# Performance work log

Measured on AMD Instinct MI355X. Metric: run time of the kernel, lower is better.

The kernel has to match this reference:

```python
import jax, jax.numpy as jnp
import numpy as np

B, S, H = 32, 256, 128
K, C, DSUB, O = 8, 4096, 16, 6  # PQ subspaces, ncentroids=4096, subvector dim, bits/symbol


def setup_inputs() -> dict:
    key = jax.random.key(0)
    ks = jax.random.split(key, 8)
    return {
        "z": jax.random.normal(ks[0], (B, S, 3), jnp.float32),
        "W1": jax.random.normal(ks[1], (3, H), jnp.float32) * 0.3,
        "b1": jax.random.normal(ks[2], (H,), jnp.float32) * 0.1,
        "W2": jax.random.normal(ks[3], (H, H), jnp.float32) * 0.1,
        "b2": jax.random.normal(ks[4], (H,), jnp.float32) * 0.1,
        "centroids": jax.random.normal(ks[5], (K, C, DSUB), jnp.float32),
        "W3": jax.random.normal(ks[6], (H, O), jnp.float32) * 0.1,
        "b3": jax.random.normal(ks[7], (O,), jnp.float32) * 0.1,
    }


def reference(z, W1, b1, W2, b2, centroids, W3, b3):
    # Small demapper MLP (layers 1-2, exact dense math)
    h1 = jax.nn.relu(z @ W1 + b1)            # [B,S,H]
    h2 = jax.nn.relu(h1 @ W2 + b2)           # [B,S,H] == layer3in
    N = B * S
    x = h2.reshape(N, K, DSUB)               # split rows into K PQ subvectors
    # Encode: nearest centroid per subspace (||x-c||^2 argmin; ||x||^2 is constant per row)
    dots = jnp.einsum("nkd,kcd->nkc", x, centroids)      # [N,K,C]
    c_norm = jnp.sum(centroids * centroids, axis=-1)      # [K,C]
    codes = jnp.argmin(c_norm[None, :, :] - 2.0 * dots, axis=-1)  # [N,K] int
    # LUT: precomputed centroid @ W3 per subspace
    W3r = W3.reshape(K, DSUB, O)
    lut = jnp.einsum("kcd,kdo->kco", centroids, W3r)      # [K,C,O]
    # Approximate matmul: sum of LUT entries selected by codes
    approx = jnp.sum(lut[jnp.arange(K)[None, :], codes], axis=1)  # [N,O]
    llr = (approx + b3).reshape(B, S * O)                 # [B, n]
    return llr
```

## Files before the change

### kernel.cpp

```cpp
#include <hip/hip_runtime.h>
#include <hip/hip_fp16.h>
#include <stdint.h>

#define NROWS 8192
#define HDIM  128
#define KSUB  8
#define NC    4096
#define DSUB  16
#define OUTD  6

#define FB_TAU 6e-5f
#define DOTSCALE (-2.0f / 4096.0f)

typedef _Float16 f16x8 __attribute__((ext_vector_type(8)));
typedef float    f32x4 __attribute__((ext_vector_type(4)));

#define XK_OFF 0u
#define CN_OFF 4194304u
#define B1_OFF 4325376u
#define PK_OFF 6422528u

__global__ __launch_bounds__(256) void prep_kernel(
    const float* __restrict__ z, const float* __restrict__ W1, const float* __restrict__ b1,
    const float* __restrict__ W2, const float* __restrict__ b2,
    const float* __restrict__ ce,
    float* __restrict__ xk, float* __restrict__ cnorm, f16x8* __restrict__ B1S)
{
    __shared__ float h1s[16 * HDIM];
    __shared__ float w2s[HDIM * HDIM];
    const int t = threadIdx.x;
    const int row0 = blockIdx.x * 16;

    {
        const int e = blockIdx.x * 256 + t;
        const int k    = e >> 14;
        const int tile = (e >> 6) & 255;
        const int lane = e & 63;
        const int col  = lane & 15;
        const int quad = lane >> 4;
        const int dims = (quad & 1) * 8;
        const int part = quad >> 1;
        const int n = tile * 16 + col;
        const float* cp = &ce[((size_t)k * NC + n) * DSUB + dims];
        f16x8 hi, lo;
        #pragma unroll
        for (int j = 0; j < 8; ++j) {
            const float s = cp[j] * 16.0f;
            const _Float16 h = (_Float16)s;
            hi[j] = h;
            lo[j] = (_Float16)(s - (float)h);
        }
        B1S[e] = part ? lo : hi;
    }

    if (blockIdx.x < (KSUB * NC) / 256) {
        const int g = blockIdx.x * 256 + t;
        const float4* cp = (const float4*)&ce[(size_t)g * DSUB];
        float nn = 0.f;
        #pragma unroll
        for (int q = 0; q < 4; ++q) {
            const float4 v = cp[q];
            nn = fmaf(v.x, v.x, nn); nn = fmaf(v.y, v.y, nn);
            nn = fmaf(v.z, v.z, nn); nn = fmaf(v.w, v.w, nn);
        }
        cnorm[g] = nn;
    }

    {
        const float4* g4 = (const float4*)W2;
        float4* s4 = (float4*)w2s;
        #pragma unroll
        for (int q = 0; q < 16; ++q) s4[t + q * 256] = g4[t + q * 256];
    }

    #pragma unroll
    for (int e = 0; e < 8; ++e) {
        const int idx = e * 256 + t;
        const int r = idx >> 7, j = idx & 127;
        const int n = row0 + r;
        float acc = b1[j];
        acc = fmaf(z[n * 3 + 0], W1[0 * HDIM + j], acc);
        acc = fmaf(z[n * 3 + 1], W1[1 * HDIM + j], acc);
        acc = fmaf(z[n * 3 + 2], W1[2 * HDIM + j], acc);
        h1s[idx] = fmaxf(acc, 0.f);
    }
    __syncthreads();

    const int c4 = (t & 31) * 4;
    const int r2 = (t >> 5) * 2;
    float acc[2][4];
    #pragma unroll
    for (int a = 0; a < 2; ++a)
        #pragma unroll
        for (int b = 0; b < 4; ++b) acc[a][b] = 0.f;

    for (int k4 = 0; k4 < HDIM; k4 += 4) {
        float hh[2][4], ww[4][4];
        #pragma unroll
        for (int q = 0; q < 2; ++q) {
            const float4 v = *(const float4*)&h1s[(r2 + q) * HDIM + k4];
            hh[q][0] = v.x; hh[q][1] = v.y; hh[q][2] = v.z; hh[q][3] = v.w;
        }
        #pragma unroll
        for (int p = 0; p < 4; ++p) {
            const float4 v = *(const float4*)&w2s[(k4 + p) * HDIM + c4];
            ww[p][0] = v.x; ww[p][1] = v.y; ww[p][2] = v.z; ww[p][3] = v.w;
        }
        #pragma unroll
        for (int q = 0; q < 2; ++q)
            #pragma unroll
            for (int p = 0; p < 4; ++p) {
                acc[q][0] = fmaf(hh[q][p], ww[p][0], acc[q][0]);
                acc[q][1] = fmaf(hh[q][p], ww[p][1], acc[q][1]);
                acc[q][2] = fmaf(hh[q][p], ww[p][2], acc[q][2]);
                acc[q][3] = fmaf(hh[q][p], ww[p][3], acc[q][3]);
            }
    }

    const float4 bb = *(const float4*)&b2[c4];
    const int kk = c4 >> 4;
    const int dd = c4 & 15;
    #pragma unroll
    for (int q = 0; q < 2; ++q) {
        float4 o;
        o.x = fmaxf(acc[q][0] + bb.x, 0.f);
        o.y = fmaxf(acc[q][1] + bb.y, 0.f);
        o.z = fmaxf(acc[q][2] + bb.z, 0.f);
        o.w = fmaxf(acc[q][3] + bb.w, 0.f);
        *(float4*)&xk[((size_t)kk * NROWS + (row0 + r2 + q)) * DSUB + dd] = o;
    }
}

__global__ __launch_bounds__(256, 8) void argmin_kernel(
    const float* __restrict__ xk, const f16x8* __restrict__ B1S,
    const float* __restrict__ cnorm, unsigned long long* __restrict__ pk)
{
    __shared__ f16x8 cs[8 * 64];
    __shared__ float cnL[1024];
    const int t = threadIdx.x;
    const int lane = t & 63;
    const int wid  = t >> 6;
    const int k  = blockIdx.y;
    const int cz = blockIdx.z;
    const int rb = blockIdx.x * 4 + wid;
    const int col  = lane & 15;
    const int quad = lane >> 4;
    const int dims = (quad & 1) * 8;
    const int part = quad >> 1;

    {
        const float* cnp0 = &cnorm[k * NC + cz * 1024];
        #pragma unroll
        for (int q = 0; q < 4; ++q) cnL[t + q * 256] = cnp0[t + q * 256];
    }

    f16x8 A[2];
    #pragma unroll
    for (int g = 0; g < 2; ++g) {
        const int row = rb * 32 + g * 16 + col;
        const float* xp = &xk[((size_t)k * NROWS + row) * DSUB + dims];
        f16x8 hi, lo;
        #pragma unroll
        for (int j = 0; j < 8; ++j) {
            const float s = xp[j] * 256.0f;
            const _Float16 h = (_Float16)s;
            hi[j] = h;
            lo[j] = (_Float16)(s - (float)h);
        }
        A[g] = part ? lo : hi;
    }

    float m1[2][4], m2[2][4];
    int   idx[2][4];
    #pragma unroll
    for (int g = 0; g < 2; ++g)
        #pragma unroll
        for (int j = 0; j < 4; ++j) { m1[g][j] = 1e30f; m2[g][j] = 1e30f; idx[g][j] = 0; }

    const f16x8* gp = &B1S[((size_t)k * 256 + cz * 64) * 64];

    for (int ch = 0; ch < 8; ++ch) {
        __syncthreads();
        {
            const uint4* g4 = (const uint4*)(gp + (size_t)ch * 512);
            uint4* s4 = (uint4*)cs;
            #pragma unroll
            for (int q = 0; q < 2; ++q) s4[t + q * 256] = g4[t + q * 256];
        }
        __syncthreads();

        #pragma unroll 2
        for (int tt = 0; tt < 8; ++tt) {
            const f16x8 b1 = cs[tt * 64 + lane];
            const f16x8 b2 = cs[tt * 64 + (lane ^ 32)];
            const float nrm = cnL[(ch * 8 + tt) * 16 + col];
            const f32x4 zz = {0.f, 0.f, 0.f, 0.f};
            f32x4 p0 = __builtin_amdgcn_mfma_f32_16x16x32_f16(A[0], b1, zz, 0, 0, 0);
            p0       = __builtin_amdgcn_mfma_f32_16x16x32_f16(A[0], b2, p0, 0, 0, 0);
            f32x4 p1 = __builtin_amdgcn_mfma_f32_16x16x32_f16(A[1], b1, zz, 0, 0, 0);
            p1       = __builtin_amdgcn_mfma_f32_16x16x32_f16(A[1], b2, p1, 0, 0, 0);
            const int c = ((cz * 64 + ch * 8 + tt) << 4) + col;
            #pragma unroll
            for (int j = 0; j < 4; ++j) {
                {
                    const float s = fmaf(p0[j], DOTSCALE, nrm);
                    const bool lt = s < m1[0][j];
                    m2[0][j] = __builtin_amdgcn_fmed3f(s, m1[0][j], m2[0][j]);
                    idx[0][j] = lt ? c : idx[0][j];
                    m1[0][j] = fminf(s, m1[0][j]);
                }
                {
                    const float s = fmaf(p1[j], DOTSCALE, nrm);
                    const bool lt = s < m1[1][j];
                    m2[1][j] = __builtin_amdgcn_fmed3f(s, m1[1][j], m2[1][j]);
                    idx[1][j] = lt ? c : idx[1][j];
                    m1[1][j] = fminf(s, m1[1][j]);
                }
            }
        }
    }

    #pragma unroll
    for (int off = 1; off < 16; off <<= 1) {
        #pragma unroll
        for (int g = 0; g < 2; ++g)
            #pragma unroll
            for (int j = 0; j < 4; ++j) {
                const float om1 = __shfl_xor(m1[g][j], off, 64);
                const float om2 = __shfl_xor(m2[g][j], off, 64);
                const int  oidx = __shfl_xor(idx[g][j], off, 64);
                const bool better = (om1 < m1[g][j]) ||
                                    (om1 == m1[g][j] && oidx < idx[g][j]);
                m2[g][j] = fminf(fminf(m2[g][j], om2), fmaxf(m1[g][j], om1));
                m1[g][j] = better ? om1 : m1[g][j];
                idx[g][j] = better ? oidx : idx[g][j];
            }
    }

    if (col == 0) {
        #pragma unroll
        for (int g = 0; g < 2; ++g)
            #pragma unroll
            for (int j = 0; j < 4; ++j) {
                const int row = rb * 32 + g * 16 + quad * 4 + j;
                unsigned u = __float_as_uint(m1[g][j]);
                u = (u & 0x80000000u) ? ~u : (u | 0x80000000u);
                const unsigned short dh =
                    __half_as_ushort(__float2half(m2[g][j] - m1[g][j]));
                pk[((size_t)cz * NROWS + row) * KSUB + k] =
                    ((unsigned long long)u << 32) |
                    ((unsigned)dh << 16) | (unsigned)idx[g][j];
            }
    }
}

__global__ __launch_bounds__(256) void finish_kernel(
    const float* __restrict__ xk, const float* __restrict__ ce,
    const float* __restrict__ cnorm, const unsigned long long* __restrict__ pk,
    const float* __restrict__ W3, const float* __restrict__ b3,
    float* __restrict__ out)
{
    __shared__ int codes_s[256];
    __shared__ int wl_s[256];
    __shared__ int wcnt;
    const int t = threadIdx.x;
    const int row0 = blockIdx.x * 32;
    if (t == 0) wcnt = 0;
    __syncthreads();

    {
        const int row = row0 + (t >> 3);
        const int k = t & 7;
        unsigned long long p[4];
        #pragma unroll
        for (int s = 0; s < 4; ++s)
            p[s] = pk[((size_t)s * NROWS + row) * KSUB + k];
        unsigned long long w = p[0];
        #pragma unroll
        for (int s = 1; s < 4; ++s) w = p[s] < w ? p[s] : w;
        const unsigned uw = (unsigned)(w >> 32);
        const float m1w = __uint_as_float((uw & 0x80000000u) ? (uw ^ 0x80000000u) : ~uw);
        float m2g = m1w + (float)__ushort_as_half((unsigned short)((unsigned)w >> 16));
        #pragma unroll
        for (int s = 0; s < 4; ++s) {
            if (p[s] != w) {
                const unsigned us = (unsigned)(p[s] >> 32);
                m2g = fminf(m2g, __uint_as_float(
                    (us & 0x80000000u) ? (us ^ 0x80000000u) : ~us));
            }
        }
        codes_s[t] = (int)(w & 0xFFFFull);
        if (m2g - m1w < FB_TAU) {
            const int slot = atomicAdd(&wcnt, 1);
            wl_s[slot] = t;
        }
    }
    __syncthreads();

    {
        const int lane = t & 63;
        const int wid = t >> 6;
        const int nitems = wcnt;
        for (int i = wid; i < nitems; i += 4) {
            const int wg = wl_s[i];
            const int row = row0 + (wg >> 3), k = wg & 7;
            float xr[DSUB];
            {
                const float* xp = &xk[((size_t)k * NROWS + row) * DSUB];
                #pragma unroll
                for (int q = 0; q < DSUB; q += 4) {
                    const float4 v = *(const float4*)&xp[q];
                    xr[q + 0] = -2.f * v.x; xr[q + 1] = -2.f * v.y;
                    xr[q + 2] = -2.f * v.z; xr[q + 3] = -2.f * v.w;
                }
            }
            float bm = 1e30f; int bi = NC;
            for (int c = lane; c < NC; c += 64) {
                const float* cp = &ce[((size_t)k * NC + c) * DSUB];
                float s = cnorm[k * NC + c];
                #pragma unroll
                for (int d = 0; d < DSUB; ++d) s = fmaf(xr[d], cp[d], s);
                if (s < bm) { bm = s; bi = c; }
            }
            #pragma unroll
            for (int off = 1; off < 64; off <<= 1) {
                const float om = __shfl_xor(bm, off, 64);
                const int  oi = __shfl_xor(bi, off, 64);
                const bool better = (om < bm) || (om == bm && oi < bi);
                bm = better ? om : bm;
                bi = better ? oi : bi;
            }
            if (lane == 0) codes_s[wg] = bi;
        }
    }
    __syncthreads();

    if (t < 32 * OUTD) {
        const int nl = t / OUTD;
        const int o = t - nl * OUTD;
        const int n = row0 + nl;
        float acc = b3[o];
        #pragma unroll
        for (int k = 0; k < KSUB; ++k) {
            const int code = codes_s[nl * KSUB + k];
            const float* cp = &ce[((size_t)k * NC + code) * DSUB];
            const float* wp = &W3[(k * DSUB) * OUTD + o];
            #pragma unroll
            for (int d = 0; d < DSUB; ++d)
                acc = fmaf(cp[d], wp[d * OUTD], acc);
        }
        out[n * OUTD + o] = acc;
    }
}

extern "C" void kernel_launch(void* const* d_in, const int* in_sizes, int n_in,
                              void* d_out, int out_size, void* d_ws, size_t ws_size,
                              hipStream_t stream)
{
    const float* z  = (const float*)d_in[0];
    const float* W1 = (const float*)d_in[1];
    const float* b1 = (const float*)d_in[2];
    const float* W2 = (const float*)d_in[3];
    const float* b2 = (const float*)d_in[4];
    const float* ce = (const float*)d_in[5];
    const float* W3 = (const float*)d_in[6];
    const float* b3 = (const float*)d_in[7];

    char* ws = (char*)d_ws;
    float* xk    = (float*)(ws + XK_OFF);
    float* cnorm = (float*)(ws + CN_OFF);
    f16x8* B1S   = (f16x8*)(ws + B1_OFF);
    unsigned long long* pk = (unsigned long long*)(ws + PK_OFF);

    hipLaunchKernelGGL(prep_kernel, dim3(512), dim3(256), 0, stream,
                       z, W1, b1, W2, b2, ce, xk, cnorm, B1S);
    hipLaunchKernelGGL(argmin_kernel, dim3(64, 8, 4), dim3(256), 0, stream,
                       xk, B1S, cnorm, pk);
    hipLaunchKernelGGL(finish_kernel, dim3(256), dim3(256), 0, stream,
                       xk, ce, cnorm, pk, W3, b3, (float*)d_out);
}
```

Baseline: 168.4 us.

## Fuse prep, argmin and finish into one kernel with last-block completion

Merges the three launches into a single kernel. Each block recomputes its slice of the MLP layers in shared memory, computes centroid norms and fp16 hi/lo splits on the fly, and the last-arriving block per row group (via an atomic counter) does the fallback and LUT output. This removes the launch gaps and intermediate global buffers. The cost is redundant layer-1/2 compute across blocks, higher shared memory use that lowers occupancy, and a serialized tail in the finishing blocks.

```diff
diff --git a/kernel.cpp b/kernel.cpp
--- a/kernel.cpp
+++ b/kernel.cpp
@@ -16,158 +16,123 @@
 typedef float    f32x4 __attribute__((ext_vector_type(4)));
 
 #define XK_OFF 0u
-#define CN_OFF 4194304u
-#define B1_OFF 4325376u
-#define PK_OFF 6422528u
-
-__global__ __launch_bounds__(256) void prep_kernel(
+#define PK_OFF 4194304u
+#define DN_OFF 6291456u
+
+#define SM_TOTAL 50176
+#define X2_OFF_B 33792
+#define W2_OFF_B 41984
+
+__global__ __launch_bounds__(256, 3) void fused_kernel(
     const float* __restrict__ z, const float* __restrict__ W1, const float* __restrict__ b1,
     const float* __restrict__ W2, const float* __restrict__ b2,
-    const float* __restrict__ ce,
-    float* __restrict__ xk, float* __restrict__ cnorm, f16x8* __restrict__ B1S)
+    const float* __restrict__ ce, const float* __restrict__ W3, const float* __restrict__ b3,
+    float* __restrict__ xk, unsigned long long* __restrict__ pk,
+    unsigned int* __restrict__ done, float* __restrict__ out)
 {
-    __shared__ float h1s[16 * HDIM];
-    __shared__ float w2s[HDIM * HDIM];
-    const int t = threadIdx.x;
-    const int row0 = blockIdx.x * 16;
-
-    {
-        const int e = blockIdx.x * 256 + t;
-        const int k    = e >> 14;
-        const int tile = (e >> 6) & 255;
-        const int lane = e & 63;
-        const int col  = lane & 15;
-        const int quad = lane >> 4;
-        const int dims = (quad & 1) * 8;
-        const int part = quad >> 1;
-        const int n = tile * 16 + col;
-        const float* cp = &ce[((size_t)k * NC + n) * DSUB + dims];
-        f16x8 hi, lo;
-        #pragma unroll
-        for (int j = 0; j < 8; ++j) {
-            const float s = cp[j] * 16.0f;
-            const _Float16 h = (_Float16)s;
-            hi[j] = h;
-            lo[j] = (_Float16)(s - (float)h);
-        }
-        B1S[e] = part ? lo : hi;
-    }
-
-    if (blockIdx.x < (KSUB * NC) / 256) {
-        const int g = blockIdx.x * 256 + t;
-        const float4* cp = (const float4*)&ce[(size_t)g * DSUB];
-        float nn = 0.f;
-        #pragma unroll
-        for (int q = 0; q < 4; ++q) {
-            const float4 v = cp[q];
-            nn = fmaf(v.x, v.x, nn); nn = fmaf(v.y, v.y, nn);
-            nn = fmaf(v.z, v.z, nn); nn = fmaf(v.w, v.w, nn);
-        }
-        cnorm[g] = nn;
-    }
-
-    {
-        const float4* g4 = (const float4*)W2;
-        float4* s4 = (float4*)w2s;
-        #pragma unroll
-        for (int q = 0; q < 16; ++q) s4[t + q * 256] = g4[t + q * 256];
-    }
-
-    #pragma unroll
-    for (int e = 0; e < 8; ++e) {
-        const int idx = e * 256 + t;
-        const int r = idx >> 7, j = idx & 127;
-        const int n = row0 + r;
-        float acc = b1[j];
-        acc = fmaf(z[n * 3 + 0], W1[0 * HDIM + j], acc);
-        acc = fmaf(z[n * 3 + 1], W1[1 * HDIM + j], acc);
-        acc = fmaf(z[n * 3 + 2], W1[2 * HDIM + j], acc);
-        h1s[idx] = fmaxf(acc, 0.f);
-    }
-    __syncthreads();
-
-    const int c4 = (t & 31) * 4;
-    const int r2 = (t >> 5) * 2;
-    float acc[2][4];
-    #pragma unroll
-    for (int a = 0; a < 2; ++a)
-        #pragma unroll
-        for (int b = 0; b < 4; ++b) acc[a][b] = 0.f;
-
-    for (int k4 = 0; k4 < HDIM; k4 += 4) {
-        float hh[2][4], ww[4][4];
-        #pragma unroll
-        for (int q = 0; q < 2; ++q) {
-            const float4 v = *(const float4*)&h1s[(r2 + q) * HDIM + k4];
-            hh[q][0] = v.x; hh[q][1] = v.y; hh[q][2] = v.z; hh[q][3] = v.w;
-        }
-        #pragma unroll
-        for (int p = 0; p < 4; ++p) {
-            const float4 v = *(const float4*)&w2s[(k4 + p) * HDIM + c4];
-            ww[p][0] = v.x; ww[p][1] = v.y; ww[p][2] = v.z; ww[p][3] = v.w;
-        }
-        #pragma unroll
-        for (int q = 0; q < 2; ++q)
-            #pragma unroll
-            for (int p = 0; p < 4; ++p) {
-                acc[q][0] = fmaf(hh[q][p], ww[p][0], acc[q][0]);
-                acc[q][1] = fmaf(hh[q][p], ww[p][1], acc[q][1]);
-                acc[q][2] = fmaf(hh[q][p], ww[p][2], acc[q][2]);
-                acc[q][3] = fmaf(hh[q][p], ww[p][3], acc[q][3]);
-            }
-    }
-
-    const float4 bb = *(const float4*)&b2[c4];
-    const int kk = c4 >> 4;
-    const int dd = c4 & 15;
-    #pragma unroll
-    for (int q = 0; q < 2; ++q) {
-        float4 o;
-        o.x = fmaxf(acc[q][0] + bb.x, 0.f);
-        o.y = fmaxf(acc[q][1] + bb.y, 0.f);
-        o.z = fmaxf(acc[q][2] + bb.z, 0.f);
-        o.w = fmaxf(acc[q][3] + bb.w, 0.f);
-        *(float4*)&xk[((size_t)kk * NROWS + (row0 + r2 + q)) * DSUB + dd] = o;
-    }
-}
-
-__global__ __launch_bounds__(256, 8) void argmin_kernel(
-    const float* __restrict__ xk, const f16x8* __restrict__ B1S,
-    const float* __restrict__ cnorm, unsigned long long* __restrict__ pk)
-{
-    __shared__ f16x8 cs[8 * 64];
-    __shared__ float cnL[1024];
+    __shared__ __align__(16) char smem[SM_TOTAL];
+    float* h1s = (float*)smem;
+    float* x2s = (float*)(smem + X2_OFF_B);
+    float* w2k = (float*)(smem + W2_OFF_B);
+    f16x8* cs  = (f16x8*)smem;
+    float* cnL = (float*)(smem + 8192);
+    int* codes_s = (int*)smem;
+    int* wl_s    = (int*)(smem + 4096);
+    __shared__ int wcnt;
+    __shared__ int isLast;
+
     const int t = threadIdx.x;
     const int lane = t & 63;
     const int wid  = t >> 6;
+    const int bx = blockIdx.x;
     const int k  = blockIdx.y;
     const int cz = blockIdx.z;
-    const int rb = blockIdx.x * 4 + wid;
+    const int row0 = bx * 128;
+
+    #pragma unroll
+    for (int q = 0; q < 8; ++q) {
+        const int e = q * 256 + t;
+        w2k[e] = W2[(e >> 4) * HDIM + k * DSUB + (e & 15)];
+    }
+
+    for (int h = 0; h < 2; ++h) {
+        __syncthreads();
+        #pragma unroll
+        for (int q = 0; q < 32; ++q) {
+            const int e = q * 256 + t;
+            const int r = e >> 7, j = e & 127;
+            const int n = row0 + h * 64 + r;
+            float a = b1[j];
+            a = fmaf(z[n * 3 + 0], W1[0 * HDIM + j], a);
+            a = fmaf(z[n * 3 + 1], W1[1 * HDIM + j], a);
+            a = fmaf(z[n * 3 + 2], W1[2 * HDIM + j], a);
+            h1s[r * 132 + j] = fmaxf(a, 0.f);
+        }
+        __syncthreads();
+        {
+            const int r  = t >> 2;
+            const int c0 = (t & 3) * 4;
+            float a0 = 0.f, a1 = 0.f, a2 = 0.f, a3 = 0.f;
+            for (int k4 = 0; k4 < HDIM; k4 += 4) {
+                const float4 hh = *(const float4*)&h1s[r * 132 + k4];
+                const float* wp = &w2k[k4 * 16 + c0];
+                a0 = fmaf(hh.x, wp[0],  a0); a1 = fmaf(hh.x, wp[1],  a1);
+                a2 = fmaf(hh.x, wp[2],  a2); a3 = fmaf(hh.x, wp[3],  a3);
+                a0 = fmaf(hh.y, wp[16], a0); a1 = fmaf(hh.y, wp[17], a1);
+                a2 = fmaf(hh.y, wp[18], a2); a3 = fmaf(hh.y, wp[19], a3);
+                a0 = fmaf(hh.z, wp[32], a0); a1 = fmaf(hh.z, wp[33], a1);
+                a2 = fmaf(hh.z, wp[34], a2); a3 = fmaf(hh.z, wp[35], a3);
+                a0 = fmaf(hh.w, wp[48], a0); a1 = fmaf(hh.w, wp[49], a1);
+                a2 = fmaf(hh.w, wp[50], a2); a3 = fmaf(hh.w, wp[51], a3);
+            }
+            const float4 bb = *(const float4*)&b2[k * DSUB + c0];
+            float4 o;
+            o.x = fmaxf(a0 + bb.x, 0.f);
+            o.y = fmaxf(a1 + bb.y, 0.f);
+            o.z = fmaxf(a2 + bb.z, 0.f);
+            o.w = fmaxf(a3 + bb.w, 0.f);
+            *(float4*)&x2s[(h * 64 + r) * 16 + c0] = o;
+        }
+    }
+    __syncthreads();
+
     const int col  = lane & 15;
     const int quad = lane >> 4;
     const int dims = (quad & 1) * 8;
     const int part = quad >> 1;
-
-    {
-        const float* cnp0 = &cnorm[k * NC + cz * 1024];
-        #pragma unroll
-        for (int q = 0; q < 4; ++q) cnL[t + q * 256] = cnp0[t + q * 256];
-    }
-
     f16x8 A[2];
     #pragma unroll
     for (int g = 0; g < 2; ++g) {
-        const int row = rb * 32 + g * 16 + col;
-        const float* xp = &xk[((size_t)k * NROWS + row) * DSUB + dims];
+        const float* xp = &x2s[(wid * 32 + g * 16 + col) * 16 + dims];
         f16x8 hi, lo;
         #pragma unroll
         for (int j = 0; j < 8; ++j) {
             const float s = xp[j] * 256.0f;
-            const _Float16 h = (_Float16)s;
-            hi[j] = h;
-            lo[j] = (_Float16)(s - (float)h);
+            const _Float16 hh = (_Float16)s;
+            hi[j] = hh;
+            lo[j] = (_Float16)(s - (float)hh);
         }
         A[g] = part ? lo : hi;
+    }
+    if (cz == 0) {
+        #pragma unroll
+        for (int q = 0; q < 2; ++q) {
+            const int e = q * 256 + t;
+            ((float4*)&xk[((size_t)k * NROWS + row0) * DSUB])[e] = ((float4*)x2s)[e];
+        }
+    }
+    #pragma unroll
+    for (int q = 0; q < 4; ++q) {
+        const int cl = q * 256 + t;
+        const float4* cp = (const float4*)&ce[((size_t)k * NC + cz * 1024 + cl) * DSUB];
+        float nn = 0.f;
+        #pragma unroll
+        for (int qq = 0; qq < 4; ++qq) {
+            const float4 v = cp[qq];
+            nn = fmaf(v.x, v.x, nn); nn = fmaf(v.y, v.y, nn);
+            nn = fmaf(v.z, v.z, nn); nn = fmaf(v.w, v.w, nn);
+        }
+        cnL[cl] = nn;
     }
 
     float m1[2][4], m2[2][4];
@@ -177,28 +142,39 @@
         #pragma unroll
         for (int j = 0; j < 4; ++j) { m1[g][j] = 1e30f; m2[g][j] = 1e30f; idx[g][j] = 0; }
 
-    const f16x8* gp = &B1S[((size_t)k * 256 + cz * 64) * 64];
-
     for (int ch = 0; ch < 8; ++ch) {
         __syncthreads();
-        {
-            const uint4* g4 = (const uint4*)(gp + (size_t)ch * 512);
-            uint4* s4 = (uint4*)cs;
-            #pragma unroll
-            for (int q = 0; q < 2; ++q) s4[t + q * 256] = g4[t + q * 256];
+        #pragma unroll
+        for (int q = 0; q < 2; ++q) {
+            const int e  = q * 256 + t;
+            const int tl = e >> 6, le = e & 63;
+            const int n  = (cz * 64 + ch * 8 + tl) * 16 + (le & 15);
+            const float* cp = &ce[((size_t)k * NC + n) * DSUB + ((le >> 4) & 1) * 8];
+            const float4 va = *(const float4*)cp;
+            const float4 vb = *(const float4*)(cp + 4);
+            const float sv[8] = {va.x, va.y, va.z, va.w, vb.x, vb.y, vb.z, vb.w};
+            f16x8 hi, lo;
+            #pragma unroll
+            for (int j = 0; j < 8; ++j) {
+                const float s = sv[j] * 16.0f;
+                const _Float16 hh = (_Float16)s;
+                hi[j] = hh;
+                lo[j] = (_Float16)(s - (float)hh);
+            }
+            cs[e] = (le >> 5) ? lo : hi;
         }
         __syncthreads();
 
         #pragma unroll 2
         for (int tt = 0; tt < 8; ++tt) {
-            const f16x8 b1 = cs[tt * 64 + lane];
-            const f16x8 b2 = cs[tt * 64 + (lane ^ 32)];
+            const f16x8 b1f = cs[tt * 64 + lane];
+            const f16x8 b2f = cs[tt * 64 + (lane ^ 32)];
             const float nrm = cnL[(ch * 8 + tt) * 16 + col];
             const f32x4 zz = {0.f, 0.f, 0.f, 0.f};
-            f32x4 p0 = __builtin_amdgcn_mfma_f32_16x16x32_f16(A[0], b1, zz, 0, 0, 0);
-            p0       = __builtin_amdgcn_mfma_f32_16x16x32_f16(A[0], b2, p0, 0, 0, 0);
-            f32x4 p1 = __builtin_amdgcn_mfma_f32_16x16x32_f16(A[1], b1, zz, 0, 0, 0);
-            p1       = __builtin_amdgcn_mfma_f32_16x16x32_f16(A[1], b2, p1, 0, 0, 0);
+            f32x4 p0 = __builtin_amdgcn_mfma_f32_16x16x32_f16(A[0], b1f, zz, 0, 0, 0);
+            p0       = __builtin_amdgcn_mfma_f32_16x16x32_f16(A[0], b2f, p0, 0, 0, 0);
+            f32x4 p1 = __builtin_amdgcn_mfma_f32_16x16x32_f16(A[1], b1f, zz, 0, 0, 0);
+            p1       = __builtin_amdgcn_mfma_f32_16x16x32_f16(A[1], b2f, p1, 0, 0, 0);
             const int c = ((cz * 64 + ch * 8 + tt) << 4) + col;
             #pragma unroll
             for (int j = 0; j < 4; ++j) {
@@ -242,7 +218,7 @@
         for (int g = 0; g < 2; ++g)
             #pragma unroll
             for (int j = 0; j < 4; ++j) {
-                const int row = rb * 32 + g * 16 + quad * 4 + j;
+                const int row = row0 + wid * 32 + g * 16 + quad * 4 + j;
                 unsigned u = __float_as_uint(m1[g][j]);
                 u = (u & 0x80000000u) ? ~u : (u | 0x80000000u);
                 const unsigned short dh =
@@ -252,29 +228,25 @@
                     ((unsigned)dh << 16) | (unsigned)idx[g][j];
             }
     }
-}
-
-__global__ __launch_bounds__(256) void finish_kernel(
-    const float* __restrict__ xk, const float* __restrict__ ce,
-    const float* __restrict__ cnorm, const unsigned long long* __restrict__ pk,
-    const float* __restrict__ W3, const float* __restrict__ b3,
-    float* __restrict__ out)
-{
-    __shared__ int codes_s[256];
-    __shared__ int wl_s[256];
-    __shared__ int wcnt;
-    const int t = threadIdx.x;
-    const int row0 = blockIdx.x * 32;
+
+    __threadfence();
+    __syncthreads();
+    if (t == 0) isLast = (atomicAdd(&done[bx], 1u) == 31u) ? 1 : 0;
+    __syncthreads();
+    if (!isLast) return;
+    __threadfence();
+
     if (t == 0) wcnt = 0;
     __syncthreads();
 
-    {
-        const int row = row0 + (t >> 3);
-        const int k = t & 7;
+    #pragma unroll
+    for (int i = 0; i < 4; ++i) {
+        const int pr = i * 256 + t;
+        const int row = row0 + (pr >> 3), kk = pr & 7;
         unsigned long long p[4];
         #pragma unroll
         for (int s = 0; s < 4; ++s)
-            p[s] = pk[((size_t)s * NROWS + row) * KSUB + k];
+            p[s] = pk[((size_t)s * NROWS + row) * KSUB + kk];
         unsigned long long w = p[0];
         #pragma unroll
         for (int s = 1; s < 4; ++s) w = p[s] < w ? p[s] : w;
@@ -289,24 +261,19 @@
                     (us & 0x80000000u) ? (us ^ 0x80000000u) : ~us));
             }
         }
-        codes_s[t] = (int)(w & 0xFFFFull);
-        if (m2g - m1w < FB_TAU) {
-            const int slot = atomicAdd(&wcnt, 1);
-            wl_s[slot] = t;
-        }
+        codes_s[pr] = (int)(w & 0xFFFFull);
+        if (m2g - m1w < FB_TAU) wl_s[atomicAdd(&wcnt, 1)] = pr;
     }
     __syncthreads();
 
     {
-        const int lane = t & 63;
-        const int wid = t >> 6;
-        const int nitems = wcnt;
-        for (int i = wid; i < nitems; i += 4) {
-            const int wg = wl_s[i];
-            const int row = row0 + (wg >> 3), k = wg & 7;
+        const int nit = wcnt;
+        for (int i = wid; i < nit; i += 4) {
+            const int pr = wl_s[i];
+            const int row = row0 + (pr >> 3), kk = pr & 7;
             float xr[DSUB];
             {
-                const float* xp = &xk[((size_t)k * NROWS + row) * DSUB];
+                const float* xp = &xk[((size_t)kk * NROWS + row) * DSUB];
                 #pragma unroll
                 for (int q = 0; q < DSUB; q += 4) {
                     const float4 v = *(const float4*)&xp[q];
@@ -316,10 +283,26 @@
             }
             float bm = 1e30f; int bi = NC;
             for (int c = lane; c < NC; c += 64) {
-                const float* cp = &ce[((size_t)k * NC + c) * DSUB];
-                float s = cnorm[k * NC + c];
-                #pragma unroll
-                for (int d = 0; d < DSUB; ++d) s = fmaf(xr[d], cp[d], s);
+                const float4* cp = (const float4*)&ce[((size_t)kk * NC + c) * DSUB];
+                const float4 v0 = cp[0], v1 = cp[1], v2 = cp[2], v3 = cp[3];
+                float nn = 0.f;
+                nn = fmaf(v0.x, v0.x, nn); nn = fmaf(v0.y, v0.y, nn);
+                nn = fmaf(v0.z, v0.z, nn); nn = fmaf(v0.w, v0.w, nn);
+                nn = fmaf(v1.x, v1.x, nn); nn = fmaf(v1.y, v1.y, nn);
+                nn = fmaf(v1.z, v1.z, nn); nn = fmaf(v1.w, v1.w, nn);
+                nn = fmaf(v2.x, v2.x, nn); nn = fmaf(v2.y, v2.y, nn);
+                nn = fmaf(v2.z, v2.z, nn); nn = fmaf(v2.w, v2.w, nn);
+                nn = fmaf(v3.x, v3.x, nn); nn = fmaf(v3.y, v3.y, nn);
+                nn = fmaf(v3.z, v3.z, nn); nn = fmaf(v3.w, v3.w, nn);
+                float s = nn;
+                s = fmaf(xr[0],  v0.x, s); s = fmaf(xr[1],  v0.y, s);
+                s = fmaf(xr[2],  v0.z, s); s = fmaf(xr[3],  v0.w, s);
+                s = fmaf(xr[4],  v1.x, s); s = fmaf(xr[5],  v1.y, s);
+                s = fmaf(xr[6],  v1.z, s); s = fmaf(xr[7],  v1.w, s);
+                s = fmaf(xr[8],  v2.x, s); s = fmaf(xr[9],  v2.y, s);
+                s = fmaf(xr[10], v2.z, s); s = fmaf(xr[11], v2.w, s);
+                s = fmaf(xr[12], v3.x, s); s = fmaf(xr[13], v3.y, s);
+                s = fmaf(xr[14], v3.z, s); s = fmaf(xr[15], v3.w, s);
                 if (s < bm) { bm = s; bi = c; }
             }
             #pragma unroll
@@ -330,26 +313,30 @@
                 bm = better ? om : bm;
                 bi = better ? oi : bi;
             }
-            if (lane == 0) codes_s[wg] = bi;
-        }
-    }
-    __syncthreads();
-
-    if (t < 32 * OUTD) {
-        const int nl = t / OUTD;
-        const int o = t - nl * OUTD;
-        const int n = row0 + nl;
-        float acc = b3[o];
-        #pragma unroll
-        for (int k = 0; k < KSUB; ++k) {
-            const int code = codes_s[nl * KSUB + k];
-            const float* cp = &ce[((size_t)k * NC + code) * DSUB];
-            const float* wp = &W3[(k * DSUB) * OUTD + o];
-            #pragma unroll
-            for (int d = 0; d < DSUB; ++d)
-                acc = fmaf(cp[d], wp[d * OUTD], acc);
-        }
-        out[n * OUTD + o] = acc;
+            if (lane == 0) codes_s[pr] = bi;
+        }
+    }
+    __syncthreads();
+
+    #pragma unroll
+    for (int i = 0; i < 3; ++i) {
+        const int e = i * 256 + t;
+        if (e < 128 * OUTD) {
+            const int nl = e / OUTD;
+            const int o = e - nl * OUTD;
+            const int n = row0 + nl;
+            float a = b3[o];
+            #pragma unroll
+            for (int kk = 0; kk < KSUB; ++kk) {
+                const int code = codes_s[nl * KSUB + kk];
+                const float* cp = &ce[((size_t)kk * NC + code) * DSUB];
+                const float* wp = &W3[(kk * DSUB) * OUTD + o];
+                #pragma unroll
+                for (int d = 0; d < DSUB; ++d)
+                    a = fmaf(cp[d], wp[d * OUTD], a);
+            }
+            out[n * OUTD + o] = a;
+        }
     }
 }
 
@@ -367,15 +354,12 @@
     const float* b3 = (const float*)d_in[7];
 
     char* ws = (char*)d_ws;
-    float* xk    = (float*)(ws + XK_OFF);
-    float* cnorm = (float*)(ws + CN_OFF);
-    f16x8* B1S   = (f16x8*)(ws + B1_OFF);
+    float* xk = (float*)(ws + XK_OFF);
     unsigned long long* pk = (unsigned long long*)(ws + PK_OFF);
-
-    hipLaunchKernelGGL(prep_kernel, dim3(512), dim3(256), 0, stream,
-                       z, W1, b1, W2, b2, ce, xk, cnorm, B1S);
-    hipLaunchKernelGGL(argmin_kernel, dim3(64, 8, 4), dim3(256), 0, stream,
-                       xk, B1S, cnorm, pk);
-    hipLaunchKernelGGL(finish_kernel, dim3(256), dim3(256), 0, stream,
-                       xk, ce, cnorm, pk, W3, b3, (float*)d_out);
+    unsigned int* done = (unsigned int*)(ws + DN_OFF);
+
+    hipMemsetAsync(done, 0, 64 * sizeof(unsigned int), stream);
+    hipLaunchKernelGGL(fused_kernel, dim3(64, 8, 4), dim3(256), 0, stream,
+                       z, W1, b1, W2, b2, ce, W3, b3,
+                       xk, pk, done, (float*)d_out);
 }
```

Result: slower. 392.4 us (+133.0%).
